# Performance work log

Hardware: AMD Instinct MI355X
Metric: run time of the kernel (lower is better)

Reference implementation:

```python
import jax, jax.numpy as jnp
import numpy as np

B = 256      # batch
ZD = 128     # z_dim
HIN = 128    # H_inputs
H = 512      # hidden
HT = 32      # H_t
N = 16384    # num nodes
RW = 16      # rw_len
TEMP = 1.0
P_DROP = 0.2
EPS_C = 0.1  # constraints epsilon


def setup_inputs() -> dict:
    key = jax.random.key(0)
    ks = jax.random.split(key, 20)
    def w(k, shape, fan):
        return (jax.random.normal(k, shape, jnp.float32) / np.float32(np.sqrt(fan)))
    z = lambda n: jnp.zeros((n,), jnp.float32)
    u = jax.random.uniform(ks[14], (RW, B, N), jnp.float32)
    return {
        "latent": jax.random.normal(ks[0], (B, ZD + 1), jnp.float32),
        "inputs0": jnp.zeros((B, HIN), jnp.float32),
        "Wc": w(ks[1], (ZD, ZD + 1), ZD + 1), "bc": z(ZD),
        "Ws": w(ks[2], (H, ZD), ZD), "bs": z(H),
        "Wh": w(ks[3], (H, H), H), "bh": z(H),
        "Wcc": w(ks[4], (H, H), H), "bcc": z(H),
        "W_ih": w(ks[5], (4 * H, HIN), HIN), "b_ih": z(4 * H),
        "W_hh": w(ks[6], (4 * H, H), H), "b_hh": z(4 * H),
        "W_up": w(ks[7], (N, H), H), "b_up": z(N),
        "W_down": w(ks[8], (HIN, N), N),
        "Wt_down": w(ks[9], (HT, H), H), "bt_down": z(HT),
        "Wt_pred": w(ks[10], (1, HT), HT),
        "Wt_up": w(ks[11], (HT, 1), 1), "bt_up": z(HT),
        "W_vt": w(ks[12], (HIN, HIN + HT), HIN + HT),
        "W_prob": w(ks[13], (1, HIN), HIN),
        # pre-sampled Gumbel noise per step (torch.rand -> gumbel)
        "gumbel": -jnp.log(-jnp.log(u + 1e-20) + 1e-20),
        # uniforms for dropout masks in TimeDecoder (forced train mode)
        "drop_u": jax.random.uniform(ks[15], (RW, B, HT), jnp.float32),
    }


def reference(latent, inputs0, Wc, bc, Ws, bs, Wh, bh, Wcc, bcc,
              W_ih, b_ih, W_hh, b_hh, W_up, b_up, W_down,
              Wt_down, bt_down, Wt_pred, Wt_up, bt_up, W_vt, W_prob,
              gumbel, drop_u):
    # induced=True path: compress latent, init (h, c)
    lat = jnp.tanh(latent @ Wc.T + bc)               # [B, ZD]
    s = jnp.tanh(lat @ Ws.T + bs)                    # [B, H]
    h0 = jnp.tanh(s @ Wh.T + bh)
    c0 = jnp.tanh(s @ Wcc.T + bcc)
    keep = 1.0 - P_DROP

    def step(carry, xs):
        x, h, c, last_t = carry
        g, du = xs
        # torch LSTMCell: gate order i, f, g, o
        gates = x @ W_ih.T + b_ih + h @ W_hh.T + b_hh  # [B, 4H]
        i, f, gg, o = jnp.split(gates, 4, axis=1)
        c2 = jax.nn.sigmoid(f) * c + jax.nn.sigmoid(i) * jnp.tanh(gg)
        h2 = jax.nn.sigmoid(o) * jnp.tanh(c2)
        # node logits + gumbel-softmax sample
        p = h2 @ W_up.T + b_up                         # [B, N]
        v = jax.nn.softmax((p + g) / TEMP, axis=1)
        Hg = v @ W_down.T                              # [B, HIN]
        # TimeDecoder (dropout always in train mode)
        td = jnp.tanh(h2 @ Wt_down.T + bt_down)        # [B, HT]
        td = td * (du < keep).astype(td.dtype) / keep
        t = jnp.minimum(td @ Wt_pred.T, 1.0)           # [B, 1]
        # constraints(t, last_t)
        mn = jnp.min(t)
        t = jnp.where(mn < EPS_C, t - mn, t)
        mx = jnp.max(t)
        t = jnp.where(mx > 1.0, t / mx, t)
        t = jnp.clip(t, last_t, 1.0)
        Ht = t @ Wt_up.T + bt_up                       # [B, HT]
        x2 = jnp.concatenate([Hg, Ht], axis=1) @ W_vt.T  # [B, HIN]
        return (x2, h2, c2, t), (v, t)

    last_t0 = jnp.zeros((latent.shape[0], 1), latent.dtype)
    (xf, _, _, _), (rw, ts) = jax.lax.scan(step, (inputs0, h0, c0, last_t0), (gumbel, drop_u))
    rw = jnp.transpose(rw, (1, 0, 2))   # [B, RW, N]
    ts = jnp.transpose(ts, (1, 0, 2))   # [B, RW, 1]
    prob = xf @ W_prob.T                # [B, 1]
    return rw, ts, prob
```

## Files before the change

kernel.cpp:

```cpp
#include <hip/hip_runtime.h>

typedef float  __attribute__((ext_vector_type(4))) f32x4;
typedef int    __attribute__((ext_vector_type(4))) i32x4;
typedef unsigned short u16;

#define B    256
#define H    512
#define HIN  128
#define N    16384
#define RW   16
#define HT   32
#define KC2  672
#define HOFF 160
#define RWN  262144
#define TS_OFF   67108864
#define PROB_OFF 67112960

__device__ __forceinline__ u16 f2bf(float f) {
  unsigned u = __builtin_bit_cast(unsigned, f);
  u += 0x7FFFu + ((u >> 16) & 1u);
  return (u16)(u >> 16);
}
__device__ __forceinline__ float bf2f(u16 v) {
  return __builtin_bit_cast(float, ((unsigned)v) << 16);
}
__device__ __forceinline__ float sigm(float x) { return 1.0f / (1.0f + expf(-x)); }

__device__ __forceinline__ void mfma(f32x4& d, i32x4 a, i32x4 b) {
  asm volatile("v_mfma_f32_16x16x32_bf16 %0, %1, %2, %0" : "+v"(d) : "v"(a), "v"(b));
}
__device__ __forceinline__ void mfma_n(f32x4& d, i32x4 a, i32x4 b) {
  asm volatile("s_nop 1\n\tv_mfma_f32_16x16x32_bf16 %0, %1, %2, %0" : "+v"(d) : "v"(a), "v"(b));
}
__device__ __forceinline__ void fence_acc(f32x4& v) {
  asm volatile("s_nop 7\n\ts_nop 7" : "+v"(v));
}

__global__ __launch_bounds__(256) void k_prep(
    const float* __restrict__ W_up, const float* __restrict__ W_down,
    const float* __restrict__ W_hh, const float* __restrict__ Wt_down,
    const float* __restrict__ b_ih, const float* __restrict__ b_hh,
    const float* __restrict__ Wh, const float* __restrict__ Wcc,
    u16* __restrict__ Wup_b, u16* __restrict__ Wdn_b, u16* __restrict__ Wfull,
    u16* __restrict__ Wtd_b, u16* __restrict__ Whc_b,
    float* __restrict__ bcomb, u16* __restrict__ xcat0, float* __restrict__ tstep)
{
  const int idx0 = blockIdx.x * 256 + threadIdx.x;
  const int stride = gridDim.x * 256;
  for (int i = idx0; i < N * H; i += stride) Wup_b[i] = f2bf(W_up[i]);
  for (int i = idx0; i < HIN * N; i += stride) Wdn_b[i] = f2bf(W_down[i]);
  for (int i = idx0; i < 4 * H * H; i += stride) {
    int j = i >> 9, k = i & 511;
    Wfull[j * KC2 + HOFF + k] = f2bf(W_hh[i]);
  }
  for (int i = idx0; i < HT * H; i += stride) Wtd_b[i] = f2bf(Wt_down[i]);
  for (int i = idx0; i < 2 * H * H; i += stride) {
    int j = i >> 9, k = i & 511;
    Whc_b[i] = f2bf(j < H ? Wh[j * H + k] : Wcc[(j - H) * H + k]);
  }
  for (int i = idx0; i < 4 * H; i += stride) bcomb[i] = b_ih[i] + b_hh[i];
  for (int i = idx0; i < B * HOFF; i += stride) {
    int b = i / HOFF, m = i - b * HOFF;
    xcat0[b * KC2 + m] = 0;
  }
  for (int i = idx0; i < B; i += stride) tstep[i] = 0.0f;
}

__global__ __launch_bounds__(256) void k_fold(
    const float* __restrict__ W_ih, const float* __restrict__ W_vt,
    const float* __restrict__ inputs0, const float* __restrict__ W_prob,
    u16* __restrict__ Wfull, float* __restrict__ g0add, float* __restrict__ wpc)
{
  int idx = blockIdx.x * 256 + threadIdx.x;
  if (idx < 2048 * 160) {
    int j = idx / 160, m = idx - j * 160;
    float a = 0.0f;
    for (int c = 0; c < HIN; ++c) a += W_ih[j * HIN + c] * W_vt[c * 160 + m];
    Wfull[j * KC2 + m] = f2bf(a);
  } else if (idx < 2048 * 160 + 256 * 2048) {
    int i2 = idx - 2048 * 160;
    int b = i2 >> 11, j = i2 & 2047;
    float a = 0.0f;
    for (int k = 0; k < HIN; ++k) a += inputs0[b * HIN + k] * W_ih[j * HIN + k];
    g0add[i2] = a;
  } else if (idx < 2048 * 160 + 256 * 2048 + 160) {
    int m = idx - (2048 * 160 + 256 * 2048);
    float a = 0.0f;
    for (int k = 0; k < HIN; ++k) a += W_prob[k] * W_vt[k * 160 + m];
    wpc[m] = a;
  }
}

__global__ __launch_bounds__(256) void k_lat(
    const float* __restrict__ latent, const float* __restrict__ Wc,
    const float* __restrict__ bc, float* __restrict__ latbuf)
{
  int idx = blockIdx.x * 256 + threadIdx.x;
  int b = idx >> 7, i = idx & 127;
  float acc = bc[i];
  for (int k = 0; k < 129; ++k) acc += latent[b * 129 + k] * Wc[i * 129 + k];
  latbuf[idx] = tanhf(acc);
}

__global__ __launch_bounds__(256) void k_sinit(
    const float* __restrict__ latbuf, const float* __restrict__ Ws,
    const float* __restrict__ bs, u16* __restrict__ sinit_b)
{
  int idx = blockIdx.x * 256 + threadIdx.x;
  int b = idx >> 9, j = idx & 511;
  float acc = bs[j];
  for (int k = 0; k < HIN; ++k) acc += latbuf[b * HIN + k] * Ws[j * HIN + k];
  sinit_b[idx] = f2bf(tanhf(acc));
}

__global__ __launch_bounds__(256) void k_h0c0m(
    const u16* __restrict__ sinit_b, const u16* __restrict__ Whc_b,
    const float* __restrict__ bh, const float* __restrict__ bcc,
    float* __restrict__ cbuf, u16* __restrict__ xc0)
{
  const int rb = blockIdx.x >> 6, cb = blockIdx.x & 63;
  const int wave = threadIdx.x >> 6, lane = threadIdx.x & 63;
  const int lr = lane & 15, lk = lane >> 4;
  const int m0 = rb * 16, col0 = cb * 16;
  const u16* ab = sinit_b + (m0 + lr) * H + wave * 128 + 8 * lk;
  const u16* bb = Whc_b + (col0 + lr) * H + wave * 128 + 8 * lk;
  f32x4 acc[2] = {};
  mfma_n(acc[0], *(const i32x4*)(ab),      *(const i32x4*)(bb));
  mfma_n(acc[1], *(const i32x4*)(ab + 32), *(const i32x4*)(bb + 32));
  mfma(acc[0], *(const i32x4*)(ab + 64), *(const i32x4*)(bb + 64));
  mfma(acc[1], *(const i32x4*)(ab + 96), *(const i32x4*)(bb + 96));
  fence_acc(acc[0]); fence_acc(acc[1]);
  __shared__ float q[4][16][17];
  #pragma unroll
  for (int rr = 0; rr < 4; ++rr)
    q[wave][4 * lk + rr][lr] = acc[0][rr] + acc[1][rr];
  __syncthreads();
  const int r2 = threadIdx.x >> 4, jj = threadIdx.x & 15;
  float s = q[0][r2][jj] + q[1][r2][jj] + q[2][r2][jj] + q[3][r2][jj];
  int col = col0 + jj;
  if (col < H) xc0[(m0 + r2) * KC2 + HOFF + col] = f2bf(tanhf(s + bh[col]));
  else         cbuf[(m0 + r2) * H + col - H]     = tanhf(s + bcc[col - H]);
}

__global__ __launch_bounds__(256) void k_lstm(
    const u16* __restrict__ xc, const u16* __restrict__ Wfull,
    const float* __restrict__ bcomb, float* __restrict__ cbuf,
    u16* __restrict__ xn, const float* __restrict__ g0, float* __restrict__ rowL)
{
  if (blockIdx.x == 0) rowL[threadIdx.x] = 0.0f;
  const int rb = blockIdx.x >> 5, cb = blockIdx.x & 31;
  const int wave = threadIdx.x >> 6, lane = threadIdx.x & 63;
  const int lr = lane & 15, lk = lane >> 4;
  const int m0 = rb * 16, j0 = cb * 16;
  const int gcol = wave * H + j0 + lr;
  f32x4 acc[2] = {};
  const u16* brow = Wfull + gcol * KC2 + 8 * lk;
  const u16* arow = xc + (m0 + lr) * KC2 + 8 * lk;
  mfma_n(acc[0], *(const i32x4*)(arow),      *(const i32x4*)(brow));
  mfma_n(acc[1], *(const i32x4*)(arow + 32), *(const i32x4*)(brow + 32));
  #pragma unroll 4
  for (int i = 2; i < 21; ++i) {
    int kk = i * 32;
    mfma(acc[i & 1], *(const i32x4*)(arow + kk), *(const i32x4*)(brow + kk));
  }
  fence_acc(acc[0]); fence_acc(acc[1]);
  __shared__ float q[4][16][17];
  float bias = bcomb[gcol];
  #pragma unroll
  for (int rr = 0; rr < 4; ++rr)
    q[wave][4 * lk + rr][lr] = acc[0][rr] + acc[1][rr] + bias;
  __syncthreads();
  const int r2 = threadIdx.x >> 4, jj = threadIdx.x & 15;
  const int b = m0 + r2, j = j0 + jj;
  float gi = q[0][r2][jj], gf = q[1][r2][jj], gg = q[2][r2][jj], go = q[3][r2][jj];
  if (g0) {
    const float* gp = g0 + b * 2048 + j;
    gi += gp[0]; gf += gp[512]; gg += gp[1024]; go += gp[1536];
  }
  float c  = cbuf[b * H + j];
  float c2 = sigm(gf) * c + sigm(gi) * tanhf(gg);
  float h2 = sigm(go) * tanhf(c2);
  cbuf[b * H + j] = c2;
  xn[b * KC2 + HOFF + j] = f2bf(h2);
}

__global__ __launch_bounds__(256) void k_pgemm(
    const u16* __restrict__ xin, const u16* __restrict__ Wup,
    const float* __restrict__ b_up, const float* __restrict__ gum,
    float* __restrict__ out_rw, float* __restrict__ rowL,
    u16* __restrict__ HgPart, const u16* __restrict__ Wdn,
    const u16* __restrict__ Wtd, const float* __restrict__ bt_down,
    const float* __restrict__ Wt_pred, const float* __restrict__ du,
    float* __restrict__ t0, int r)
{
  const int rb = blockIdx.x >> 7, cb = blockIdx.x & 127;
  const int wave = threadIdx.x >> 6, lane = threadIdx.x & 63;
  const int lr = lane & 15, lk = lane >> 4;
  const int m0 = rb * 32;
  const int n0 = cb * 128 + wave * 32;

  float gv[2][4][2], bup0 = b_up[n0 + lr], bup1 = b_up[n0 + 16 + lr];
  #pragma unroll
  for (int mi = 0; mi < 2; ++mi)
    #pragma unroll
    for (int rr = 0; rr < 4; ++rr) {
      int row = m0 + 16 * mi + 4 * lk + rr;
      gv[mi][rr][0] = gum[(size_t)row * N + n0 + lr];
      gv[mi][rr][1] = gum[(size_t)row * N + n0 + 16 + lr];
    }

  f32x4 acc[2][2] = {};
  const u16* a0 = xin + (m0 + lr) * KC2 + HOFF + 8 * lk;
  const u16* a1 = a0 + 16 * KC2;
  const u16* b0 = Wup + (n0 + lr) * H + 8 * lk;
  const u16* b1 = b0 + 16 * H;
  {
    i32x4 af0 = *(const i32x4*)(a0);
    i32x4 af1 = *(const i32x4*)(a1);
    i32x4 bf0 = *(const i32x4*)(b0);
    i32x4 bf1 = *(const i32x4*)(b1);
    mfma_n(acc[0][0], af0, bf0); mfma_n(acc[0][1], af0, bf1);
    mfma_n(acc[1][0], af1, bf0); mfma_n(acc[1][1], af1, bf1);
  }
  #pragma unroll 3
  for (int kk = 32; kk < H; kk += 32) {
    i32x4 af0 = *(const i32x4*)(a0 + kk);
    i32x4 af1 = *(const i32x4*)(a1 + kk);
    i32x4 bf0 = *(const i32x4*)(b0 + kk);
    i32x4 bf1 = *(const i32x4*)(b1 + kk);
    mfma(acc[0][0], af0, bf0); mfma(acc[0][1], af0, bf1);
    mfma(acc[1][0], af1, bf0); mfma(acc[1][1], af1, bf1);
  }
  #pragma unroll
  for (int mi = 0; mi < 2; ++mi) { fence_acc(acc[mi][0]); fence_acc(acc[mi][1]); }

  __shared__ float eL[32][132];
  __shared__ float sL[4][32];
  #pragma unroll
  for (int mi = 0; mi < 2; ++mi)
    #pragma unroll
    for (int rr = 0; rr < 4; ++rr) {
      int rl = 16 * mi + 4 * lk + rr;
      int row = m0 + rl;
      float* sp = out_rw + (size_t)row * RWN + (size_t)r * N + n0 + lr;
      float v0 = acc[mi][0][rr] + bup0 + gv[mi][rr][0];
      float v1 = acc[mi][1][rr] + bup1 + gv[mi][rr][1];
      float e0 = expf(fminf(v0, 80.0f));
      float e1 = expf(fminf(v1, 80.0f));
      sp[0] = e0; sp[16] = e1;
      eL[rl][wave * 32 + lr] = e0;
      eL[rl][wave * 32 + 16 + lr] = e1;
      float par = e0 + e1;
      #pragma unroll
      for (int off = 1; off < 16; off <<= 1) par += __shfl_xor(par, off);
      if (lr == 0) sL[wave][rl] = par;
    }
  __syncthreads();
  if (threadIdx.x < 32)
    atomicAdd(rowL + m0 + threadIdx.x,
              sL[0][threadIdx.x] + sL[1][threadIdx.x] + sL[2][threadIdx.x] + sL[3][threadIdx.x]);

  const int nb = cb * 128;
  f32x4 acc2[2][2] = {};
  #pragma unroll
  for (int kk2 = 0; kk2 < 4; ++kk2) {
    i32x4 af[2];
    #pragma unroll
    for (int mi2 = 0; mi2 < 2; ++mi2) {
      const float* ep = &eL[16 * mi2 + lr][kk2 * 32 + 8 * lk];
      f32x4 x0 = *(const f32x4*)ep;
      f32x4 x1 = *(const f32x4*)(ep + 4);
      af[mi2][0] = (int)f2bf(x0[0]) | ((int)f2bf(x0[1]) << 16);
      af[mi2][1] = (int)f2bf(x0[2]) | ((int)f2bf(x0[3]) << 16);
      af[mi2][2] = (int)f2bf(x1[0]) | ((int)f2bf(x1[1]) << 16);
      af[mi2][3] = (int)f2bf(x1[2]) | ((int)f2bf(x1[3]) << 16);
    }
    i32x4 bf0 = *(const i32x4*)(Wdn + (size_t)(wave * 32 + lr) * N + nb + kk2 * 32 + 8 * lk);
    i32x4 bf1 = *(const i32x4*)(Wdn + (size_t)(wave * 32 + 16 + lr) * N + nb + kk2 * 32 + 8 * lk);
    mfma_n(acc2[0][0], af[0], bf0); mfma_n(acc2[0][1], af[0], bf1);
    mfma_n(acc2[1][0], af[1], bf0); mfma_n(acc2[1][1], af[1], bf1);
  }
  #pragma unroll
  for (int mi2 = 0; mi2 < 2; ++mi2) { fence_acc(acc2[mi2][0]); fence_acc(acc2[mi2][1]); }
  u16* hp = HgPart + (size_t)cb * (B * HIN);
  #pragma unroll
  for (int mi2 = 0; mi2 < 2; ++mi2)
    #pragma unroll
    for (int ni = 0; ni < 2; ++ni)
      #pragma unroll
      for (int rr = 0; rr < 4; ++rr)
        hp[(m0 + 16 * mi2 + 4 * lk + rr) * HIN + wave * 32 + 16 * ni + lr] =
            f2bf(acc2[mi2][ni][rr]);

  if (cb == 0 && wave < 2) {
    f32x4 acc3[2] = {};
    const u16* at = xin + (m0 + wave * 16 + lr) * KC2 + HOFF + 8 * lk;
    {
      i32x4 af = *(const i32x4*)(at);
      mfma_n(acc3[0], af, *(const i32x4*)(Wtd + lr * H + 8 * lk));
      mfma_n(acc3[1], af, *(const i32x4*)(Wtd + (16 + lr) * H + 8 * lk));
    }
    for (int kk = 32; kk < H; kk += 32) {
      i32x4 af = *(const i32x4*)(at + kk);
      mfma(acc3[0], af, *(const i32x4*)(Wtd + lr * H + kk + 8 * lk));
      mfma(acc3[1], af, *(const i32x4*)(Wtd + (16 + lr) * H + kk + 8 * lk));
    }
    fence_acc(acc3[0]); fence_acc(acc3[1]);
    float wp0 = Wt_pred[lr],  wp1 = Wt_pred[16 + lr];
    float bt0 = bt_down[lr],  bt1 = bt_down[16 + lr];
    #pragma unroll
    for (int rr = 0; rr < 4; ++rr) {
      int row = m0 + wave * 16 + 4 * lk + rr;
      float td0 = tanhf(acc3[0][rr] + bt0);
      float td1 = tanhf(acc3[1][rr] + bt1);
      td0 = (du[row * HT + lr]      < 0.8f) ? td0 * 1.25f : 0.0f;
      td1 = (du[row * HT + 16 + lr] < 0.8f) ? td1 * 1.25f : 0.0f;
      float part = td0 * wp0 + td1 * wp1;
      #pragma unroll
      for (int off = 1; off < 16; off <<= 1) part += __shfl_xor(part, off);
      if (lr == 0) t0[row] = fminf(part, 1.0f);
    }
  }
}

__global__ __launch_bounds__(256) void k_vscale(
    float* __restrict__ out_rw, const float* __restrict__ rowL,
    const u16* __restrict__ HgPart, const float* __restrict__ t0,
    float* __restrict__ tstep, const float* __restrict__ Wt_up,
    const float* __restrict__ bt_up, float* __restrict__ ts_out,
    u16* __restrict__ xn, float* __restrict__ Hgf, int r)
{
  const int b = blockIdx.x, tid = threadIdx.x;
  const int rg = b >> 7, cb = b & 127;
  const int row = rg * 16 + (tid >> 4);
  const int coff = (tid & 15) * 8;
  const float R = 1.0f / rowL[row];
  float* orow = out_rw + (size_t)row * RWN + (size_t)r * N + cb * 128 + coff;
  f32x4 x0 = *(const f32x4*)orow;
  f32x4 x1 = *(const f32x4*)(orow + 4);
  #pragma unroll
  for (int e = 0; e < 4; ++e) { x0[e] *= R; x1[e] *= R; }
  *(f32x4*)orow = x0;
  *(f32x4*)(orow + 4) = x1;

  if ((b & 15) == 8) {
    const int idx = (b >> 4) * 256 + tid;
    float s0 = 0.f, s1 = 0.f, s2 = 0.f, s3 = 0.f;
    #pragma unroll 4
    for (int c = 0; c < 128; c += 4) {
      s0 += bf2f(HgPart[(size_t)(c + 0) * (B * HIN) + idx]);
      s1 += bf2f(HgPart[(size_t)(c + 1) * (B * HIN) + idx]);
      s2 += bf2f(HgPart[(size_t)(c + 2) * (B * HIN) + idx]);
      s3 += bf2f(HgPart[(size_t)(c + 3) * (B * HIN) + idx]);
    }
    float hg = ((s0 + s1) + (s2 + s3)) / rowL[idx >> 7];
    Hgf[idx] = hg;
    xn[(idx >> 7) * KC2 + (idx & 127)] = f2bf(hg);
  }

  if (b == 2047) {
    __shared__ float red[256];
    float tv = t0[tid];
    red[tid] = tv; __syncthreads();
    for (int s = 128; s > 0; s >>= 1) {
      if (tid < s) red[tid] = fminf(red[tid], red[tid + s]);
      __syncthreads();
    }
    float mn = red[0]; __syncthreads();
    if (mn < 0.1f) tv -= mn;
    red[tid] = tv; __syncthreads();
    for (int s = 128; s > 0; s >>= 1) {
      if (tid < s) red[tid] = fmaxf(red[tid], red[tid + s]);
      __syncthreads();
    }
    float mx = red[0];
    if (mx > 1.0f) tv /= mx;
    tv = fminf(fmaxf(tv, tstep[r * B + tid]), 1.0f);
    tstep[(r + 1) * B + tid] = tv;
    ts_out[tid * RW + r] = tv;
    #pragma unroll 4
    for (int j = 0; j < HT; ++j)
      xn[tid * KC2 + HIN + j] = f2bf(tv * Wt_up[j] + bt_up[j]);
  }
}

__global__ __launch_bounds__(256) void k_prob(
    const float* __restrict__ Hgf, const float* __restrict__ tstep,
    const float* __restrict__ Wt_up, const float* __restrict__ bt_up,
    const float* __restrict__ wpc, float* __restrict__ outp)
{
  int b = threadIdx.x;
  float acc = 0.0f;
  for (int m = 0; m < HIN; ++m) acc += Hgf[b * HIN + m] * wpc[m];
  float tv = tstep[16 * B + b];
  for (int j = 0; j < HT; ++j) acc += (tv * Wt_up[j] + bt_up[j]) * wpc[HIN + j];
  outp[b] = acc;
}

extern "C" void kernel_launch(void* const* d_in, const int* in_sizes, int n_in,
                              void* d_out, int out_size, void* d_ws, size_t ws_size,
                              hipStream_t stream) {
  (void)in_sizes; (void)n_in; (void)out_size; (void)ws_size;
  const float* latent  = (const float*)d_in[0];
  const float* inputs0 = (const float*)d_in[1];
  const float* Wc      = (const float*)d_in[2];
  const float* bc      = (const float*)d_in[3];
  const float* Ws      = (const float*)d_in[4];
  const float* bs      = (const float*)d_in[5];
  const float* Wh      = (const float*)d_in[6];
  const float* bh      = (const float*)d_in[7];
  const float* Wcc     = (const float*)d_in[8];
  const float* bcc     = (const float*)d_in[9];
  const float* W_ih    = (const float*)d_in[10];
  const float* b_ih    = (const float*)d_in[11];
  const float* W_hh    = (const float*)d_in[12];
  const float* b_hh    = (const float*)d_in[13];
  const float* W_up    = (const float*)d_in[14];
  const float* b_up    = (const float*)d_in[15];
  const float* W_down  = (const float*)d_in[16];
  const float* Wt_down = (const float*)d_in[17];
  const float* bt_down = (const float*)d_in[18];
  const float* Wt_pred = (const float*)d_in[19];
  const float* Wt_up   = (const float*)d_in[20];
  const float* bt_up   = (const float*)d_in[21];
  const float* W_vt    = (const float*)d_in[22];
  const float* W_prob  = (const float*)d_in[23];
  const float* gumbel  = (const float*)d_in[24];
  const float* drop_u  = (const float*)d_in[25];
  float* out = (float*)d_out;

  char* p = (char*)d_ws;
  auto alloc = [&](size_t bytes) { char* r = p; p += (bytes + 255) & ~(size_t)255; return r; };
  u16*   Wup_b  = (u16*)  alloc((size_t)N * H * 2);
  u16*   Wdn_b  = (u16*)  alloc((size_t)HIN * N * 2);
  u16*   Wfull_b= (u16*)  alloc((size_t)4 * H * KC2 * 2);
  u16*   Wtd_b  = (u16*)  alloc((size_t)HT * H * 2);
  u16*   Whc_b  = (u16*)  alloc((size_t)2 * H * H * 2);
  float* bcomb  = (float*)alloc(4 * H * 4);
  u16*   xcat0  = (u16*)  alloc((size_t)B * KC2 * 2);
  u16*   xcat1  = (u16*)  alloc((size_t)B * KC2 * 2);
  float* cbuf   = (float*)alloc((size_t)B * H * 4);
  u16*   sinit_b= (u16*)  alloc((size_t)B * H * 2);
  float* latbuf = (float*)alloc((size_t)B * HIN * 4);
  float* rowL   = (float*)alloc(B * 4);
  float* t0buf  = (float*)alloc(B * 4);
  float* tstep  = (float*)alloc((size_t)17 * B * 4);
  u16*   HgPart = (u16*)  alloc((size_t)128 * B * HIN * 2);
  float* Hgf    = (float*)alloc((size_t)B * HIN * 4);
  float* g0add  = (float*)alloc((size_t)B * 4 * H * 4);
  float* wpc    = (float*)alloc(160 * 4);

  k_prep<<<2048, 256, 0, stream>>>(W_up, W_down, W_hh, Wt_down, b_ih, b_hh, Wh, Wcc,
                                   Wup_b, Wdn_b, Wfull_b, Wtd_b, Whc_b, bcomb, xcat0, tstep);
  k_fold<<<3330, 256, 0, stream>>>(W_ih, W_vt, inputs0, W_prob, Wfull_b, g0add, wpc);
  k_lat  <<<128, 256, 0, stream>>>(latent, Wc, bc, latbuf);
  k_sinit<<<512, 256, 0, stream>>>(latbuf, Ws, bs, sinit_b);
  k_h0c0m<<<1024, 256, 0, stream>>>(sinit_b, Whc_b, bh, bcc, cbuf, xcat0);

  for (int r = 0; r < 16; ++r) {
    u16* xc = (r & 1) ? xcat1 : xcat0;
    u16* xn = (r & 1) ? xcat0 : xcat1;
    k_lstm <<<512, 256, 0, stream>>>(xc, Wfull_b, bcomb, cbuf, xn,
                                     r == 0 ? g0add : (const float*)nullptr, rowL);
    k_pgemm<<<1024, 256, 0, stream>>>(xn, Wup_b, b_up, gumbel + (size_t)r * B * N,
                                      out, rowL, HgPart, Wdn_b,
                                      Wtd_b, bt_down, Wt_pred, drop_u + (size_t)r * B * HT,
                                      t0buf, r);
    k_vscale<<<2048, 256, 0, stream>>>(out, rowL, HgPart, t0buf, tstep, Wt_up, bt_up,
                                       out + TS_OFF, xn, Hgf, r);
  }
  k_prob<<<1, 256, 0, stream>>>(Hgf, tstep, Wt_up, bt_up, wpc, out + PROB_OFF);
}
```

Measured before the change: 1.294 ms.

## Fuse softmax normalize and Hg/time reduction into next LSTM kernel via bf16 exp buffer

The separate per-step vscale kernel is removed. The p-GEMM now writes unnormalized exponentials to a bf16 scratch buffer instead of fp32 into the output. The next step's LSTM kernel normalizes that buffer into the output, reduces HgPart, applies the time constraints, and builds the x input in shared memory. A tail kernel handles the last step. This cuts one launch per step and the fp32 read-modify-write pass over the large output. In exchange it adds redundant per-block reductions and rounds the exponentials to bf16 before normalization, which lowers precision.

```diff
diff --git a/kernel.cpp b/kernel.cpp
--- a/kernel.cpp
+++ b/kernel.cpp
@@ -3,6 +3,7 @@
 typedef float  __attribute__((ext_vector_type(4))) f32x4;
 typedef int    __attribute__((ext_vector_type(4))) i32x4;
 typedef unsigned short u16;
+typedef unsigned long long u64;
 
 #define B    256
 #define H    512
@@ -11,7 +12,6 @@
 #define RW   16
 #define HT   32
 #define KC2  672
-#define HOFF 160
 #define RWN  262144
 #define TS_OFF   67108864
 #define PROB_OFF 67112960
@@ -43,7 +43,7 @@
     const float* __restrict__ Wh, const float* __restrict__ Wcc,
     u16* __restrict__ Wup_b, u16* __restrict__ Wdn_b, u16* __restrict__ Wfull,
     u16* __restrict__ Wtd_b, u16* __restrict__ Whc_b,
-    float* __restrict__ bcomb, u16* __restrict__ xcat0, float* __restrict__ tstep)
+    float* __restrict__ bcomb, float* __restrict__ tstep, float* __restrict__ rowLs)
 {
   const int idx0 = blockIdx.x * 256 + threadIdx.x;
   const int stride = gridDim.x * 256;
@@ -51,7 +51,7 @@
   for (int i = idx0; i < HIN * N; i += stride) Wdn_b[i] = f2bf(W_down[i]);
   for (int i = idx0; i < 4 * H * H; i += stride) {
     int j = i >> 9, k = i & 511;
-    Wfull[j * KC2 + HOFF + k] = f2bf(W_hh[i]);
+    Wfull[j * KC2 + 160 + k] = f2bf(W_hh[i]);
   }
   for (int i = idx0; i < HT * H; i += stride) Wtd_b[i] = f2bf(Wt_down[i]);
   for (int i = idx0; i < 2 * H * H; i += stride) {
@@ -59,11 +59,8 @@
     Whc_b[i] = f2bf(j < H ? Wh[j * H + k] : Wcc[(j - H) * H + k]);
   }
   for (int i = idx0; i < 4 * H; i += stride) bcomb[i] = b_ih[i] + b_hh[i];
-  for (int i = idx0; i < B * HOFF; i += stride) {
-    int b = i / HOFF, m = i - b * HOFF;
-    xcat0[b * KC2 + m] = 0;
-  }
   for (int i = idx0; i < B; i += stride) tstep[i] = 0.0f;
+  for (int i = idx0; i < 16 * B; i += stride) rowLs[i] = 0.0f;
 }
 
 __global__ __launch_bounds__(256) void k_fold(
@@ -116,7 +113,7 @@
 __global__ __launch_bounds__(256) void k_h0c0m(
     const u16* __restrict__ sinit_b, const u16* __restrict__ Whc_b,
     const float* __restrict__ bh, const float* __restrict__ bcc,
-    float* __restrict__ cbuf, u16* __restrict__ xc0)
+    float* __restrict__ cbuf, u16* __restrict__ h0out)
 {
   const int rb = blockIdx.x >> 6, cb = blockIdx.x & 63;
   const int wave = threadIdx.x >> 6, lane = threadIdx.x & 63;
@@ -138,42 +135,134 @@
   const int r2 = threadIdx.x >> 4, jj = threadIdx.x & 15;
   float s = q[0][r2][jj] + q[1][r2][jj] + q[2][r2][jj] + q[3][r2][jj];
   int col = col0 + jj;
-  if (col < H) xc0[(m0 + r2) * KC2 + HOFF + col] = f2bf(tanhf(s + bh[col]));
-  else         cbuf[(m0 + r2) * H + col - H]     = tanhf(s + bcc[col - H]);
-}
-
-__global__ __launch_bounds__(256) void k_lstm(
-    const u16* __restrict__ xc, const u16* __restrict__ Wfull,
-    const float* __restrict__ bcomb, float* __restrict__ cbuf,
-    u16* __restrict__ xn, const float* __restrict__ g0, float* __restrict__ rowL)
-{
-  if (blockIdx.x == 0) rowL[threadIdx.x] = 0.0f;
-  const int rb = blockIdx.x >> 5, cb = blockIdx.x & 31;
-  const int wave = threadIdx.x >> 6, lane = threadIdx.x & 63;
+  if (col < H) h0out[(m0 + r2) * H + col] = f2bf(tanhf(s + bh[col]));
+  else         cbuf[(m0 + r2) * H + col - H] = tanhf(s + bcc[col - H]);
+}
+
+__global__ __launch_bounds__(256) void k_lstm2(
+    const u16* __restrict__ hprev, u16* __restrict__ hcur,
+    const u16* __restrict__ Wfull, const float* __restrict__ bcomb,
+    float* __restrict__ cbuf, const float* __restrict__ g0,
+    const u16* __restrict__ HgPart, const float* __restrict__ rowLs,
+    const float* __restrict__ t0buf, float* __restrict__ tstep,
+    const float* __restrict__ Wt_up, const float* __restrict__ bt_up,
+    float* __restrict__ out, const u16* __restrict__ ebp, int r)
+{
+  const int blk = blockIdx.x, tid = threadIdx.x;
+  const int wave = tid >> 6, lane = tid & 63;
   const int lr = lane & 15, lk = lane >> 4;
+  const int rb = ((blk & 7) << 1) | ((blk >> 3) & 1);
+  const int cb = blk >> 4;
   const int m0 = rb * 16, j0 = cb * 16;
+  const float* rowLprev = rowLs + (r - 1) * B;
+
+  __shared__ u16 aT[16][168];
+  __shared__ float q[4][16][17];
+  __shared__ float redS[8];
+  __shared__ float tl[256];
+
+  float tv = 0.0f;
+  if (r > 0) {
+    tv = t0buf[tid];
+    float v = tv;
+    #pragma unroll
+    for (int off = 1; off < 64; off <<= 1) v = fminf(v, __shfl_xor(v, off));
+    if (lane == 0) redS[wave] = v;
+  }
+  __syncthreads();
+  if (r > 0) {
+    float mn = fminf(fminf(redS[0], redS[1]), fminf(redS[2], redS[3]));
+    if (mn < 0.1f) tv -= mn;
+    float v = tv;
+    #pragma unroll
+    for (int off = 1; off < 64; off <<= 1) v = fmaxf(v, __shfl_xor(v, off));
+    if (lane == 0) redS[4 + wave] = v;
+  }
+  __syncthreads();
+  if (r > 0) {
+    float mx = fmaxf(fmaxf(redS[4], redS[5]), fmaxf(redS[6], redS[7]));
+    if (mx > 1.0f) tv /= mx;
+    tv = fminf(fmaxf(tv, tstep[(r - 1) * B + tid]), 1.0f);
+    if (blk == 0) {
+      tstep[r * B + tid] = tv;
+      out[TS_OFF + tid * RW + (r - 1)] = tv;
+    }
+  }
+  tl[tid] = tv;
+
+  {
+    const int row = tid >> 4, c8 = (tid & 15) * 8;
+    if (r > 0) {
+      float s0 = 0.f, s1 = 0.f, s2 = 0.f, s3 = 0.f;
+      float s4 = 0.f, s5 = 0.f, s6 = 0.f, s7 = 0.f;
+      const u16* hp = HgPart + (size_t)(m0 + row) * HIN + c8;
+      #pragma unroll 4
+      for (int c = 0; c < 128; ++c) {
+        i32x4 pk = *(const i32x4*)(hp + (size_t)c * (B * HIN));
+        s0 += bf2f((u16)pk[0]); s1 += bf2f((u16)(pk[0] >> 16));
+        s2 += bf2f((u16)pk[1]); s3 += bf2f((u16)(pk[1] >> 16));
+        s4 += bf2f((u16)pk[2]); s5 += bf2f((u16)(pk[2] >> 16));
+        s6 += bf2f((u16)pk[3]); s7 += bf2f((u16)(pk[3] >> 16));
+      }
+      float R = 1.0f / rowLprev[m0 + row];
+      aT[row][c8 + 0] = f2bf(s0 * R); aT[row][c8 + 1] = f2bf(s1 * R);
+      aT[row][c8 + 2] = f2bf(s2 * R); aT[row][c8 + 3] = f2bf(s3 * R);
+      aT[row][c8 + 4] = f2bf(s4 * R); aT[row][c8 + 5] = f2bf(s5 * R);
+      aT[row][c8 + 6] = f2bf(s6 * R); aT[row][c8 + 7] = f2bf(s7 * R);
+    } else {
+      #pragma unroll
+      for (int e = 0; e < 8; ++e) aT[row][c8 + e] = 0;
+    }
+  }
+  __syncthreads();
+
+  for (int i2 = tid; i2 < 512; i2 += 256) {
+    int row = i2 >> 5, j = i2 & 31;
+    aT[row][128 + j] = (r > 0) ? f2bf(tl[m0 + row] * Wt_up[j] + bt_up[j]) : (u16)0;
+  }
+
+  if (r > 0) {
+    #pragma unroll
+    for (int uu = 0; uu < 8; ++uu) {
+      int flat = (blk * 2048 + uu * 256 + tid) * 4;
+      int row = flat >> 14;
+      float Rv = 1.0f / rowLprev[row];
+      u64 ev = *(const u64*)(ebp + flat);
+      f32x4 o;
+      o[0] = bf2f((u16)ev) * Rv;
+      o[1] = bf2f((u16)(ev >> 16)) * Rv;
+      o[2] = bf2f((u16)(ev >> 32)) * Rv;
+      o[3] = bf2f((u16)(ev >> 48)) * Rv;
+      *(f32x4*)(out + (size_t)row * RWN + (size_t)(r - 1) * N + (flat & (N - 1))) = o;
+    }
+  }
+  __syncthreads();
+
   const int gcol = wave * H + j0 + lr;
   f32x4 acc[2] = {};
-  const u16* brow = Wfull + gcol * KC2 + 8 * lk;
-  const u16* arow = xc + (m0 + lr) * KC2 + 8 * lk;
-  mfma_n(acc[0], *(const i32x4*)(arow),      *(const i32x4*)(brow));
-  mfma_n(acc[1], *(const i32x4*)(arow + 32), *(const i32x4*)(brow + 32));
+  const u16* brow = Wfull + (size_t)gcol * KC2 + 8 * lk;
+  const u16* aL   = &aT[lr][8 * lk];
+  const u16* arow = hprev + (m0 + lr) * H + 8 * lk;
+  mfma_n(acc[0], *(const i32x4*)(aL),       *(const i32x4*)(brow));
+  mfma_n(acc[1], *(const i32x4*)(aL + 32),  *(const i32x4*)(brow + 32));
+  mfma(acc[0], *(const i32x4*)(aL + 64),  *(const i32x4*)(brow + 64));
+  mfma(acc[1], *(const i32x4*)(aL + 96),  *(const i32x4*)(brow + 96));
+  mfma(acc[0], *(const i32x4*)(aL + 128), *(const i32x4*)(brow + 128));
   #pragma unroll 4
-  for (int i = 2; i < 21; ++i) {
+  for (int i = 5; i < 21; ++i) {
     int kk = i * 32;
-    mfma(acc[i & 1], *(const i32x4*)(arow + kk), *(const i32x4*)(brow + kk));
+    mfma(acc[i & 1], *(const i32x4*)(arow + kk - 160), *(const i32x4*)(brow + kk));
   }
   fence_acc(acc[0]); fence_acc(acc[1]);
-  __shared__ float q[4][16][17];
   float bias = bcomb[gcol];
   #pragma unroll
   for (int rr = 0; rr < 4; ++rr)
     q[wave][4 * lk + rr][lr] = acc[0][rr] + acc[1][rr] + bias;
   __syncthreads();
-  const int r2 = threadIdx.x >> 4, jj = threadIdx.x & 15;
+  const int r2 = tid >> 4, jj = tid & 15;
   const int b = m0 + r2, j = j0 + jj;
   float gi = q[0][r2][jj], gf = q[1][r2][jj], gg = q[2][r2][jj], go = q[3][r2][jj];
-  if (g0) {
+  if (r == 0) {
     const float* gp = g0 + b * 2048 + j;
     gi += gp[0]; gf += gp[512]; gg += gp[1024]; go += gp[1536];
   }
@@ -181,17 +270,17 @@
   float c2 = sigm(gf) * c + sigm(gi) * tanhf(gg);
   float h2 = sigm(go) * tanhf(c2);
   cbuf[b * H + j] = c2;
-  xn[b * KC2 + HOFF + j] = f2bf(h2);
-}
-
-__global__ __launch_bounds__(256) void k_pgemm(
-    const u16* __restrict__ xin, const u16* __restrict__ Wup,
+  hcur[b * H + j] = f2bf(h2);
+}
+
+__global__ __launch_bounds__(256) void k_pgemm2(
+    const u16* __restrict__ hb, const u16* __restrict__ Wup,
     const float* __restrict__ b_up, const float* __restrict__ gum,
-    float* __restrict__ out_rw, float* __restrict__ rowL,
+    u16* __restrict__ eb, float* __restrict__ rowL,
     u16* __restrict__ HgPart, const u16* __restrict__ Wdn,
     const u16* __restrict__ Wtd, const float* __restrict__ bt_down,
     const float* __restrict__ Wt_pred, const float* __restrict__ du,
-    float* __restrict__ t0, int r)
+    float* __restrict__ t0)
 {
   const int rb = blockIdx.x >> 7, cb = blockIdx.x & 127;
   const int wave = threadIdx.x >> 6, lane = threadIdx.x & 63;
@@ -210,9 +299,9 @@
     }
 
   f32x4 acc[2][2] = {};
-  const u16* a0 = xin + (m0 + lr) * KC2 + HOFF + 8 * lk;
-  const u16* a1 = a0 + 16 * KC2;
-  const u16* b0 = Wup + (n0 + lr) * H + 8 * lk;
+  const u16* a0 = hb + (m0 + lr) * H + 8 * lk;
+  const u16* a1 = a0 + 16 * H;
+  const u16* b0 = Wup + (size_t)(n0 + lr) * H + 8 * lk;
   const u16* b1 = b0 + 16 * H;
   {
     i32x4 af0 = *(const i32x4*)(a0);
@@ -242,12 +331,12 @@
     for (int rr = 0; rr < 4; ++rr) {
       int rl = 16 * mi + 4 * lk + rr;
       int row = m0 + rl;
-      float* sp = out_rw + (size_t)row * RWN + (size_t)r * N + n0 + lr;
+      u16* sp = eb + (size_t)row * N + n0 + lr;
       float v0 = acc[mi][0][rr] + bup0 + gv[mi][rr][0];
       float v1 = acc[mi][1][rr] + bup1 + gv[mi][rr][1];
       float e0 = expf(fminf(v0, 80.0f));
       float e1 = expf(fminf(v1, 80.0f));
-      sp[0] = e0; sp[16] = e1;
+      sp[0] = f2bf(e0); sp[16] = f2bf(e1);
       eL[rl][wave * 32 + lr] = e0;
       eL[rl][wave * 32 + 16 + lr] = e1;
       float par = e0 + e1;
@@ -294,7 +383,7 @@
 
   if (cb == 0 && wave < 2) {
     f32x4 acc3[2] = {};
-    const u16* at = xin + (m0 + wave * 16 + lr) * KC2 + HOFF + 8 * lk;
+    const u16* at = hb + (m0 + wave * 16 + lr) * H + 8 * lk;
     {
       i32x4 af = *(const i32x4*)(at);
       mfma_n(acc3[0], af, *(const i32x4*)(Wtd + lr * H + 8 * lk));
@@ -323,64 +412,64 @@
   }
 }
 
-__global__ __launch_bounds__(256) void k_vscale(
-    float* __restrict__ out_rw, const float* __restrict__ rowL,
-    const u16* __restrict__ HgPart, const float* __restrict__ t0,
-    float* __restrict__ tstep, const float* __restrict__ Wt_up,
-    const float* __restrict__ bt_up, float* __restrict__ ts_out,
-    u16* __restrict__ xn, float* __restrict__ Hgf, int r)
-{
-  const int b = blockIdx.x, tid = threadIdx.x;
-  const int rg = b >> 7, cb = b & 127;
-  const int row = rg * 16 + (tid >> 4);
-  const int coff = (tid & 15) * 8;
-  const float R = 1.0f / rowL[row];
-  float* orow = out_rw + (size_t)row * RWN + (size_t)r * N + cb * 128 + coff;
-  f32x4 x0 = *(const f32x4*)orow;
-  f32x4 x1 = *(const f32x4*)(orow + 4);
-  #pragma unroll
-  for (int e = 0; e < 4; ++e) { x0[e] *= R; x1[e] *= R; }
-  *(f32x4*)orow = x0;
-  *(f32x4*)(orow + 4) = x1;
-
-  if ((b & 15) == 8) {
-    const int idx = (b >> 4) * 256 + tid;
-    float s0 = 0.f, s1 = 0.f, s2 = 0.f, s3 = 0.f;
+__global__ __launch_bounds__(256) void k_tail(
+    float* __restrict__ out, const u16* __restrict__ eb15,
+    const float* __restrict__ rowLs, const u16* __restrict__ HgPart,
+    const float* __restrict__ t0buf, float* __restrict__ tstep,
+    float* __restrict__ Hgf)
+{
+  const int blk = blockIdx.x, tid = threadIdx.x;
+  const float* rowL15 = rowLs + 15 * B;
+  #pragma unroll
+  for (int uu = 0; uu < 4; ++uu) {
+    int flat = (blk * 1024 + uu * 256 + tid) * 4;
+    int row = flat >> 14;
+    float Rv = 1.0f / rowL15[row];
+    u64 ev = *(const u64*)(eb15 + flat);
+    f32x4 o;
+    o[0] = bf2f((u16)ev) * Rv;
+    o[1] = bf2f((u16)(ev >> 16)) * Rv;
+    o[2] = bf2f((u16)(ev >> 32)) * Rv;
+    o[3] = bf2f((u16)(ev >> 48)) * Rv;
+    *(f32x4*)(out + (size_t)row * RWN + (size_t)15 * N + (flat & (N - 1))) = o;
+  }
+  if (blk < 16) {
+    const int row = blk * 16 + (tid >> 4), c8 = (tid & 15) * 8;
+    float s[8] = {};
+    const u16* hp = HgPart + (size_t)row * HIN + c8;
     #pragma unroll 4
-    for (int c = 0; c < 128; c += 4) {
-      s0 += bf2f(HgPart[(size_t)(c + 0) * (B * HIN) + idx]);
-      s1 += bf2f(HgPart[(size_t)(c + 1) * (B * HIN) + idx]);
-      s2 += bf2f(HgPart[(size_t)(c + 2) * (B * HIN) + idx]);
-      s3 += bf2f(HgPart[(size_t)(c + 3) * (B * HIN) + idx]);
-    }
-    float hg = ((s0 + s1) + (s2 + s3)) / rowL[idx >> 7];
-    Hgf[idx] = hg;
-    xn[(idx >> 7) * KC2 + (idx & 127)] = f2bf(hg);
-  }
-
-  if (b == 2047) {
-    __shared__ float red[256];
-    float tv = t0[tid];
-    red[tid] = tv; __syncthreads();
-    for (int s = 128; s > 0; s >>= 1) {
-      if (tid < s) red[tid] = fminf(red[tid], red[tid + s]);
-      __syncthreads();
-    }
-    float mn = red[0]; __syncthreads();
+    for (int c = 0; c < 128; ++c) {
+      i32x4 pk = *(const i32x4*)(hp + (size_t)c * (B * HIN));
+      s[0] += bf2f((u16)pk[0]); s[1] += bf2f((u16)(pk[0] >> 16));
+      s[2] += bf2f((u16)pk[1]); s[3] += bf2f((u16)(pk[1] >> 16));
+      s[4] += bf2f((u16)pk[2]); s[5] += bf2f((u16)(pk[2] >> 16));
+      s[6] += bf2f((u16)pk[3]); s[7] += bf2f((u16)(pk[3] >> 16));
+    }
+    float R = 1.0f / rowL15[row];
+    #pragma unroll
+    for (int e = 0; e < 8; ++e) Hgf[row * HIN + c8 + e] = s[e] * R;
+  }
+  if (blk == 16) {
+    const int wave = tid >> 6, lane = tid & 63;
+    __shared__ float redS[8];
+    float tv = t0buf[tid];
+    float v = tv;
+    #pragma unroll
+    for (int off = 1; off < 64; off <<= 1) v = fminf(v, __shfl_xor(v, off));
+    if (lane == 0) redS[wave] = v;
+    __syncthreads();
+    float mn = fminf(fminf(redS[0], redS[1]), fminf(redS[2], redS[3]));
     if (mn < 0.1f) tv -= mn;
-    red[tid] = tv; __syncthreads();
-    for (int s = 128; s > 0; s >>= 1) {
-      if (tid < s) red[tid] = fmaxf(red[tid], red[tid + s]);
-      __syncthreads();
-    }
-    float mx = red[0];
+    v = tv;
+    #pragma unroll
+    for (int off = 1; off < 64; off <<= 1) v = fmaxf(v, __shfl_xor(v, off));
+    if (lane == 0) redS[4 + wave] = v;
+    __syncthreads();
+    float mx = fmaxf(fmaxf(redS[4], redS[5]), fmaxf(redS[6], redS[7]));
     if (mx > 1.0f) tv /= mx;
-    tv = fminf(fmaxf(tv, tstep[r * B + tid]), 1.0f);
-    tstep[(r + 1) * B + tid] = tv;
-    ts_out[tid * RW + r] = tv;
-    #pragma unroll 4
-    for (int j = 0; j < HT; ++j)
-      xn[tid * KC2 + HIN + j] = f2bf(tv * Wt_up[j] + bt_up[j]);
+    tv = fminf(fmaxf(tv, tstep[15 * B + tid]), 1.0f);
+    tstep[16 * B + tid] = tv;
+    out[TS_OFF + tid * RW + 15] = tv;
   }
 }
 
@@ -437,37 +526,42 @@
   u16*   Wtd_b  = (u16*)  alloc((size_t)HT * H * 2);
   u16*   Whc_b  = (u16*)  alloc((size_t)2 * H * H * 2);
   float* bcomb  = (float*)alloc(4 * H * 4);
-  u16*   xcat0  = (u16*)  alloc((size_t)B * KC2 * 2);
-  u16*   xcat1  = (u16*)  alloc((size_t)B * KC2 * 2);
+  u16*   hbuf0  = (u16*)  alloc((size_t)B * H * 2);
+  u16*   hbuf1  = (u16*)  alloc((size_t)B * H * 2);
   float* cbuf   = (float*)alloc((size_t)B * H * 4);
   u16*   sinit_b= (u16*)  alloc((size_t)B * H * 2);
   float* latbuf = (float*)alloc((size_t)B * HIN * 4);
-  float* rowL   = (float*)alloc(B * 4);
+  float* rowLs  = (float*)alloc((size_t)16 * B * 4);
   float* t0buf  = (float*)alloc(B * 4);
   float* tstep  = (float*)alloc((size_t)17 * B * 4);
   u16*   HgPart = (u16*)  alloc((size_t)128 * B * HIN * 2);
   float* Hgf    = (float*)alloc((size_t)B * HIN * 4);
   float* g0add  = (float*)alloc((size_t)B * 4 * H * 4);
   float* wpc    = (float*)alloc(160 * 4);
+  u16*   ebuf0  = (u16*)  alloc((size_t)B * N * 2);
+  u16*   ebuf1  = (u16*)  alloc((size_t)B * N * 2);
 
   k_prep<<<2048, 256, 0, stream>>>(W_up, W_down, W_hh, Wt_down, b_ih, b_hh, Wh, Wcc,
-                                   Wup_b, Wdn_b, Wfull_b, Wtd_b, Whc_b, bcomb, xcat0, tstep);
+                                   Wup_b, Wdn_b, Wfull_b, Wtd_b, Whc_b, bcomb,
+                                   tstep, rowLs);
   k_fold<<<3330, 256, 0, stream>>>(W_ih, W_vt, inputs0, W_prob, Wfull_b, g0add, wpc);
   k_lat  <<<128, 256, 0, stream>>>(latent, Wc, bc, latbuf);
   k_sinit<<<512, 256, 0, stream>>>(latbuf, Ws, bs, sinit_b);
-  k_h0c0m<<<1024, 256, 0, stream>>>(sinit_b, Whc_b, bh, bcc, cbuf, xcat0);
+  k_h0c0m<<<1024, 256, 0, stream>>>(sinit_b, Whc_b, bh, bcc, cbuf, hbuf1);
 
   for (int r = 0; r < 16; ++r) {
-    u16* xc = (r & 1) ? xcat1 : xcat0;
-    u16* xn = (r & 1) ? xcat0 : xcat1;
-    k_lstm <<<512, 256, 0, stream>>>(xc, Wfull_b, bcomb, cbuf, xn,
-                                     r == 0 ? g0add : (const float*)nullptr, rowL);
-    k_pgemm<<<1024, 256, 0, stream>>>(xn, Wup_b, b_up, gumbel + (size_t)r * B * N,
-                                      out, rowL, HgPart, Wdn_b,
-                                      Wtd_b, bt_down, Wt_pred, drop_u + (size_t)r * B * HT,
-                                      t0buf, r);
-    k_vscale<<<2048, 256, 0, stream>>>(out, rowL, HgPart, t0buf, tstep, Wt_up, bt_up,
-                                       out + TS_OFF, xn, Hgf, r);
-  }
+    u16* hprev = (r & 1) ? hbuf0 : hbuf1;
+    u16* hcur  = (r & 1) ? hbuf1 : hbuf0;
+    u16* eb    = (r & 1) ? ebuf1 : ebuf0;
+    u16* ebp   = (r & 1) ? ebuf0 : ebuf1;
+    k_lstm2<<<512, 256, 0, stream>>>(hprev, hcur, Wfull_b, bcomb, cbuf, g0add,
+                                     HgPart, rowLs, t0buf, tstep, Wt_up, bt_up,
+                                     out, ebp, r);
+    k_pgemm2<<<1024, 256, 0, stream>>>(hcur, Wup_b, b_up, gumbel + (size_t)r * B * N,
+                                       eb, rowLs + r * B, HgPart, Wdn_b,
+                                       Wtd_b, bt_down, Wt_pred,
+                                       drop_u + (size_t)r * B * HT, t0buf);
+  }
+  k_tail<<<1024, 256, 0, stream>>>(out, ebuf1, rowLs, HgPart, t0buf, tstep, Hgf);
   k_prob<<<1, 256, 0, stream>>>(Hgf, tstep, Wt_up, bt_up, wpc, out + PROB_OFF);
 }
```

After: 1.401 ms. 1.08x slower.
